# Kernel tuning notes

Hardware: AMD Instinct MI355X
Metric: run time of the kernel (lower is better)

## Reference

```python
import jax, jax.numpy as jnp
import numpy as np

# Elliptical structuring-element sizes (cv2.MORPH_ELLIPSE-like), per init_kwargs.
KERNEL_SIZES = [3, 5, 7]
B, C, H, W = 16, 1, 1024, 1024
_MAX_VAL = 1e4  # kornia's max_val; geodesic border padding uses +-max_val
_EPS = 1e-7     # smp DiceLoss eps


def _ellipse_offsets(k):
    """Offsets (i, j) within a k x k window where the elliptical mask is 1."""
    r = k // 2
    yy, xx = np.mgrid[-r:r + 1, -r:r + 1]
    rr = max(r, 1)
    mask = (xx / rr) ** 2 + (yy / rr) ** 2 <= 1.0 + 1e-9
    return [(i, j) for i in range(k) for j in range(k) if mask[i, j]]


def _morph(x, k, offsets, is_dilation):
    """Flat morphological dilation (max) / erosion (min) over the ellipse support.
    Matches kornia's unfold-based morphology with geodesic border handling,
    but computed as a fused running max/min over static shifted views (no unfold blow-up)."""
    pad = k // 2
    fill = -_MAX_VAL if is_dilation else _MAX_VAL
    xp = jnp.pad(x, ((0, 0), (0, 0), (pad, pad), (pad, pad)), constant_values=fill)
    h, w = x.shape[-2], x.shape[-1]
    op = jnp.maximum if is_dilation else jnp.minimum
    i0, j0 = offsets[0]
    out = xp[..., i0:i0 + h, j0:j0 + w]
    for (i, j) in offsets[1:]:
        out = op(out, xp[..., i:i + h, j:j + w])
    return out


def _dice_loss(pred, target):
    """smp.losses.DiceLoss(mode='binary', from_logits=False): reduce over dims (batch, pixels)."""
    b = pred.shape[0]
    p = pred.reshape(b, 1, -1)
    t = target.reshape(b, 1, -1)
    inter = jnp.sum(p * t, axis=(0, 2))            # [1]
    card = jnp.sum(p + t, axis=(0, 2))             # [1]
    score = 2.0 * inter / jnp.clip(card, _EPS)
    loss = (1.0 - score) * (jnp.sum(t, axis=(0, 2)) > 0)
    return jnp.mean(loss)


def setup_inputs() -> dict:
    key = jax.random.key(0)
    k1, k2 = jax.random.split(key)
    pred = jax.random.uniform(k1, (B, C, H, W), dtype=jnp.float32)
    teacher = jax.random.uniform(k2, (B, C, H, W), dtype=jnp.float32)
    return {"pred_student_prob": pred, "teacher_prob": teacher}


def reference(pred_student_prob, teacher_prob):
    teacher = jax.lax.stop_gradient(teacher_prob)  # .detach()
    total = jnp.float32(0.0)
    for k in KERNEL_SIZES:
        offs = _ellipse_offsets(k)
        obj_dil = _morph(teacher, k, offs, True)
        obj_ero = _morph(teacher, k, offs, False)
        total = total + _dice_loss(pred_student_prob, obj_dil) + _dice_loss(pred_student_prob, obj_ero)
    return total / len(KERNEL_SIZES)
```

## Files before the change

kernel.cpp:

```cpp
#include <hip/hip_runtime.h>

#define H_ 1024
#define W_ 1024
#define B_ 16
#define TH 8
#define STEPS (TH + 6)
#define GX (H_ / TH)
#define NBLK (GX * B_)
#define NACC 13
#define TROW 1032


__device__ __forceinline__ void gl2lds16(const float* g, float* l) {
  __builtin_amdgcn_global_load_lds(
      (const __attribute__((address_space(1))) void*)g,
      (__attribute__((address_space(3))) void*)l,
      16, 0, 0);
}

__global__ __launch_bounds__(256) void k_partials(const float* __restrict__ pred,
                                                  const float* __restrict__ tch,
                                                  float* __restrict__ partials) {
  __shared__ float tbuf[STEPS][TROW];
  __shared__ float red[4][NACC];

  const int tid = threadIdx.x;
  const int n     = blockIdx.y * gridDim.x + blockIdx.x;
  const int b     = n >> 7;
  const int ytile = (n & 7) * 16 + ((n >> 3) & 15);
  const int y0    = ytile * TH;
  const int x0    = tid * 4;
  const int wv    = tid >> 6;
  const float* tb = tch  + (size_t)b * (H_ * W_);
  const float* pb = pred + (size_t)b * (H_ * W_);

#pragma unroll
  for (int s = 0; s < STEPS; ++s) {
    const int t    = y0 + s - 3;
    const int trow = t < 0 ? 0 : (t >= H_ ? H_ - 1 : t);
    gl2lds16(tb + (size_t)trow * W_ + x0, &tbuf[s][4 + (wv << 8)]);
  }
  float4 pv[TH];
#pragma unroll
  for (int j = 0; j < TH; ++j)
    pv[j] = *reinterpret_cast<const float4*>(pb + (size_t)(y0 + j) * W_ + x0);

  __syncthreads();

  float acc[NACC];
#pragma unroll
  for (int j = 0; j < NACC; j++) acc[j] = 0.f;

  float h0q[7][4];
  float h3M[5][4], h3N[5][4];
  float h5M[6][4], h5N[6][4];
  float h7M[4][4], h7N[4][4];

#pragma unroll
  for (int s = 0; s < STEPS; ++s) {
    const float4* t4 = reinterpret_cast<const float4*>(&tbuf[s][x0]);
    const float4 A0 = t4[0], A1 = t4[1], A2 = t4[2];
    float a[12] = {A0.x, A0.y, A0.z, A0.w, A1.x, A1.y, A1.z, A1.w, A2.x, A2.y, A2.z, A2.w};
    if (tid == 0)   { a[0] = a[1] = a[2]  = a[3]  = a[4]; }
    if (tid == 255) { a[8] = a[9] = a[10] = a[11] = a[7]; }

    float QM[8], QN[8];
#pragma unroll
    for (int i = 1; i <= 7; ++i) {
      QM[i] = fmaxf(fmaxf(a[i], a[i + 1]), a[i + 2]);
      QN[i] = fminf(fminf(a[i], a[i + 1]), a[i + 2]);
    }
#pragma unroll
    for (int c = 0; c < 4; ++c) {
      h0q[s % 7][c] = a[c + 4];
      h3M[s % 5][c] = QM[c + 3];
      h3N[s % 5][c] = QN[c + 3];
      h5M[s % 6][c] = fmaxf(QM[c + 2], QM[c + 4]);
      h5N[s % 6][c] = fminf(QN[c + 2], QN[c + 4]);
      h7M[s % 4][c] = fmaxf(fmaxf(QM[c + 1], QM[c + 4]), a[c + 7]);
      h7N[s % 4][c] = fminf(fminf(QN[c + 1], QN[c + 4]), a[c + 7]);
    }

    if (s >= 6) {
      const float4 pq = pv[s - 6];
      const float p[4] = {pq.x, pq.y, pq.z, pq.w};
#pragma unroll
      for (int c = 0; c < 4; ++c) {
        const float d3v = fmaxf(fmaxf(h3M[(s + 2) % 5][c], h0q[(s + 3) % 7][c]), h0q[(s + 5) % 7][c]);
        const float e3v = fminf(fminf(h3N[(s + 2) % 5][c], h0q[(s + 3) % 7][c]), h0q[(s + 5) % 7][c]);

        float d5v = fmaxf(fmaxf(h5M[(s + 3) % 6][c], h3M[(s + 1) % 5][c]), h3M[(s + 3) % 5][c]);
        d5v = fmaxf(fmaxf(d5v, h0q[(s + 2) % 7][c]), h0q[(s + 6) % 7][c]);
        float e5v = fminf(fminf(h5N[(s + 3) % 6][c], h3N[(s + 1) % 5][c]), h3N[(s + 3) % 5][c]);
        e5v = fminf(fminf(e5v, h0q[(s + 2) % 7][c]), h0q[(s + 6) % 7][c]);

        float d7v = fmaxf(fmaxf(h7M[(s + 1) % 4][c], h5M[(s + 2) % 6][c]), h5M[(s + 4) % 6][c]);
        d7v = fmaxf(fmaxf(d7v, h5M[(s + 1) % 6][c]), h5M[(s + 5) % 6][c]);
        d7v = fmaxf(fmaxf(d7v, h0q[(s + 1) % 7][c]), h0q[s % 7][c]);
        float e7v = fminf(fminf(h7N[(s + 1) % 4][c], h5N[(s + 2) % 6][c]), h5N[(s + 4) % 6][c]);
        e7v = fminf(fminf(e7v, h5N[(s + 1) % 6][c]), h5N[(s + 5) % 6][c]);
        e7v = fminf(fminf(e7v, h0q[(s + 1) % 7][c]), h0q[s % 7][c]);

        acc[0]  += p[c];
        acc[1]  += d3v;  acc[2]  = fmaf(p[c], d3v, acc[2]);
        acc[3]  += e3v;  acc[4]  = fmaf(p[c], e3v, acc[4]);
        acc[5]  += d5v;  acc[6]  = fmaf(p[c], d5v, acc[6]);
        acc[7]  += e5v;  acc[8]  = fmaf(p[c], e5v, acc[8]);
        acc[9]  += d7v;  acc[10] = fmaf(p[c], d7v, acc[10]);
        acc[11] += e7v;  acc[12] = fmaf(p[c], e7v, acc[12]);
      }
    }
  }

#pragma unroll
  for (int j = 0; j < NACC; j++) {
    float v = acc[j];
#pragma unroll
    for (int off = 32; off > 0; off >>= 1) v += __shfl_down(v, off, 64);
    acc[j] = v;
  }
  const int lane = tid & 63;
  if (lane == 0) {
#pragma unroll
    for (int j = 0; j < NACC; j++) red[wv][j] = acc[j];
  }
  __syncthreads();
  if (tid == 0) {
    const int bid = n;
#pragma unroll
    for (int j = 0; j < NACC; j++)
      partials[j * NBLK + bid] = red[0][j] + red[1][j] + red[2][j] + red[3][j];
  }
}

__global__ __launch_bounds__(256) void k_final(const float* __restrict__ partials,
                                               float* __restrict__ out) {
  const int tid = threadIdx.x;
  double acc[NACC];
#pragma unroll
  for (int j = 0; j < NACC; j++) acc[j] = 0.0;
#pragma unroll
  for (int k = 0; k < NBLK / 256; k++) {
#pragma unroll
    for (int j = 0; j < NACC; j++)
      acc[j] += (double)partials[j * NBLK + tid + k * 256];
  }
#pragma unroll
  for (int j = 0; j < NACC; j++) {
#pragma unroll
    for (int off = 32; off > 0; off >>= 1) acc[j] += __shfl_down(acc[j], off, 64);
  }
  __shared__ double red[4][NACC];
  const int lane = tid & 63, wv = tid >> 6;
  if (lane == 0) {
#pragma unroll
    for (int j = 0; j < NACC; j++) red[wv][j] = acc[j];
  }
  __syncthreads();
  if (tid == 0) {
    double t_[NACC];
#pragma unroll
    for (int j = 0; j < NACC; j++) t_[j] = red[0][j] + red[1][j] + red[2][j] + red[3][j];
    const double Sp = t_[0];
    double total = 0.0;
#pragma unroll
    for (int k = 0; k < 3; k++) {
      const double Sd = t_[1 + 4 * k], Id = t_[2 + 4 * k];
      const double Se = t_[3 + 4 * k], Ie = t_[4 + 4 * k];
      double cd = Sp + Sd; if (cd < 1e-7) cd = 1e-7;
      double ce = Sp + Se; if (ce < 1e-7) ce = 1e-7;
      total += (1.0 - 2.0 * Id / cd) * (Sd > 0.0 ? 1.0 : 0.0);
      total += (1.0 - 2.0 * Ie / ce) * (Se > 0.0 ? 1.0 : 0.0);
    }
    out[0] = (float)(total / 3.0);
  }
}

extern "C" void kernel_launch(void* const* d_in, const int* in_sizes, int n_in,
                              void* d_out, int out_size, void* d_ws, size_t ws_size,
                              hipStream_t stream) {
  const float* pred = (const float*)d_in[0];
  const float* tch  = (const float*)d_in[1];
  float* partials = (float*)d_ws;

  k_partials<<<dim3(GX, B_), 256, 0, stream>>>(pred, tch, partials);
  k_final<<<1, 256, 0, stream>>>(partials, (float*)d_out);
}
```

Baseline: 147.7 us.

## Load teacher rows directly into register ring buffer, drop LDS staging

Removes the LDS staging of teacher rows and the block-wide barrier. Each of 128 threads now handles 8 columns, loading its own and neighbouring float4 halos from global memory into a 7-row register ring. The morphology switches from horizontal-first to vertical-first partial max/min. Pred rows are loaded inline instead of prefetched, and the block shrinks to 128 threads. The redundant halo loads go through cache. Register pressure from a 7x16 ring plus temporaries may hurt occupancy, and there is less latency hiding without the upfront prefetch.

After: 177.6 us. 1.2x slower.

```diff
diff --git a/kernel.cpp b/kernel.cpp
--- a/kernel.cpp
+++ b/kernel.cpp
@@ -8,106 +8,94 @@
 #define GX (H_ / TH)
 #define NBLK (GX * B_)
 #define NACC 13
-#define TROW 1032
+#define TW 8
+#define BT 128
 
 
-__device__ __forceinline__ void gl2lds16(const float* g, float* l) {
-  __builtin_amdgcn_global_load_lds(
-      (const __attribute__((address_space(1))) void*)g,
-      (__attribute__((address_space(3))) void*)l,
-      16, 0, 0);
-}
-
-__global__ __launch_bounds__(256) void k_partials(const float* __restrict__ pred,
-                                                  const float* __restrict__ tch,
-                                                  float* __restrict__ partials) {
-  __shared__ float tbuf[STEPS][TROW];
-  __shared__ float red[4][NACC];
-
+__global__ __launch_bounds__(BT) void k_partials(const float* __restrict__ pred,
+                                                 const float* __restrict__ tch,
+                                                 float* __restrict__ partials) {
   const int tid = threadIdx.x;
   const int n     = blockIdx.y * gridDim.x + blockIdx.x;
   const int b     = n >> 7;
   const int ytile = (n & 7) * 16 + ((n >> 3) & 15);
   const int y0    = ytile * TH;
-  const int x0    = tid * 4;
-  const int wv    = tid >> 6;
+  const int x0    = tid * TW;
   const float* tb = tch  + (size_t)b * (H_ * W_);
   const float* pb = pred + (size_t)b * (H_ * W_);
-
-#pragma unroll
-  for (int s = 0; s < STEPS; ++s) {
-    const int t    = y0 + s - 3;
-    const int trow = t < 0 ? 0 : (t >= H_ ? H_ - 1 : t);
-    gl2lds16(tb + (size_t)trow * W_ + x0, &tbuf[s][4 + (wv << 8)]);
-  }
-  float4 pv[TH];
-#pragma unroll
-  for (int j = 0; j < TH; ++j)
-    pv[j] = *reinterpret_cast<const float4*>(pb + (size_t)(y0 + j) * W_ + x0);
-
-  __syncthreads();
 
   float acc[NACC];
 #pragma unroll
   for (int j = 0; j < NACC; j++) acc[j] = 0.f;
 
-  float h0q[7][4];
-  float h3M[5][4], h3N[5][4];
-  float h5M[6][4], h5N[6][4];
-  float h7M[4][4], h7N[4][4];
+  float ring[7][16];
 
 #pragma unroll
   for (int s = 0; s < STEPS; ++s) {
-    const float4* t4 = reinterpret_cast<const float4*>(&tbuf[s][x0]);
-    const float4 A0 = t4[0], A1 = t4[1], A2 = t4[2];
-    float a[12] = {A0.x, A0.y, A0.z, A0.w, A1.x, A1.y, A1.z, A1.w, A2.x, A2.y, A2.z, A2.w};
-    if (tid == 0)   { a[0] = a[1] = a[2]  = a[3]  = a[4]; }
-    if (tid == 255) { a[8] = a[9] = a[10] = a[11] = a[7]; }
-
-    float QM[8], QN[8];
-#pragma unroll
-    for (int i = 1; i <= 7; ++i) {
-      QM[i] = fmaxf(fmaxf(a[i], a[i + 1]), a[i + 2]);
-      QN[i] = fminf(fminf(a[i], a[i + 1]), a[i + 2]);
-    }
-#pragma unroll
-    for (int c = 0; c < 4; ++c) {
-      h0q[s % 7][c] = a[c + 4];
-      h3M[s % 5][c] = QM[c + 3];
-      h3N[s % 5][c] = QN[c + 3];
-      h5M[s % 6][c] = fmaxf(QM[c + 2], QM[c + 4]);
-      h5N[s % 6][c] = fminf(QN[c + 2], QN[c + 4]);
-      h7M[s % 4][c] = fmaxf(fmaxf(QM[c + 1], QM[c + 4]), a[c + 7]);
-      h7N[s % 4][c] = fminf(fminf(QN[c + 1], QN[c + 4]), a[c + 7]);
+    {
+      const int t    = y0 + s - 3;
+      const int trow = t < 0 ? 0 : (t >= H_ ? H_ - 1 : t);
+      const float* tr = tb + (size_t)trow * W_ + x0;
+      const float4 v1 = *reinterpret_cast<const float4*>(tr);
+      const float4 v2 = *reinterpret_cast<const float4*>(tr + 4);
+      ring[s % 7][4]  = v1.x; ring[s % 7][5]  = v1.y; ring[s % 7][6]  = v1.z; ring[s % 7][7]  = v1.w;
+      ring[s % 7][8]  = v2.x; ring[s % 7][9]  = v2.y; ring[s % 7][10] = v2.z; ring[s % 7][11] = v2.w;
+      if (tid > 0) {
+        const float4 vl = *reinterpret_cast<const float4*>(tr - 4);
+        ring[s % 7][0] = vl.x; ring[s % 7][1] = vl.y; ring[s % 7][2] = vl.z; ring[s % 7][3] = vl.w;
+      } else {
+        ring[s % 7][0] = ring[s % 7][1] = ring[s % 7][2] = ring[s % 7][3] = v1.x;
+      }
+      if (tid < BT - 1) {
+        const float4 vr = *reinterpret_cast<const float4*>(tr + 8);
+        ring[s % 7][12] = vr.x; ring[s % 7][13] = vr.y; ring[s % 7][14] = vr.z; ring[s % 7][15] = vr.w;
+      } else {
+        ring[s % 7][12] = ring[s % 7][13] = ring[s % 7][14] = ring[s % 7][15] = v2.w;
+      }
     }
 
     if (s >= 6) {
-      const float4 pq = pv[s - 6];
-      const float p[4] = {pq.x, pq.y, pq.z, pq.w};
+      float V3M[16], V3N[16], V5M[16], V5N[16];
 #pragma unroll
-      for (int c = 0; c < 4; ++c) {
-        const float d3v = fmaxf(fmaxf(h3M[(s + 2) % 5][c], h0q[(s + 3) % 7][c]), h0q[(s + 5) % 7][c]);
-        const float e3v = fminf(fminf(h3N[(s + 2) % 5][c], h0q[(s + 3) % 7][c]), h0q[(s + 5) % 7][c]);
+      for (int i = 2; i <= 13; ++i) {
+        const float rm1 = ring[(s + 3) % 7][i], rc = ring[(s + 4) % 7][i], rp1 = ring[(s + 5) % 7][i];
+        V3M[i] = fmaxf(fmaxf(rm1, rc), rp1);
+        V3N[i] = fminf(fminf(rm1, rc), rp1);
+        V5M[i] = fmaxf(fmaxf(V3M[i], ring[(s + 2) % 7][i]), ring[(s + 6) % 7][i]);
+        V5N[i] = fminf(fminf(V3N[i], ring[(s + 2) % 7][i]), ring[(s + 6) % 7][i]);
+      }
+      const float* pr = pb + (size_t)(y0 + s - 6) * W_ + x0;
+      const float4 p1 = *reinterpret_cast<const float4*>(pr);
+      const float4 p2 = *reinterpret_cast<const float4*>(pr + 4);
+      const float p[TW] = {p1.x, p1.y, p1.z, p1.w, p2.x, p2.y, p2.z, p2.w};
+#pragma unroll
+      for (int c = 0; c < TW; ++c) {
+        const int i = c + 4;
+        const float V7M = fmaxf(fmaxf(V5M[i], ring[(s + 1) % 7][i]), ring[s % 7][i]);
+        const float V7N = fminf(fminf(V5N[i], ring[(s + 1) % 7][i]), ring[s % 7][i]);
 
-        float d5v = fmaxf(fmaxf(h5M[(s + 3) % 6][c], h3M[(s + 1) % 5][c]), h3M[(s + 3) % 5][c]);
-        d5v = fmaxf(fmaxf(d5v, h0q[(s + 2) % 7][c]), h0q[(s + 6) % 7][c]);
-        float e5v = fminf(fminf(h5N[(s + 3) % 6][c], h3N[(s + 1) % 5][c]), h3N[(s + 3) % 5][c]);
-        e5v = fminf(fminf(e5v, h0q[(s + 2) % 7][c]), h0q[(s + 6) % 7][c]);
+        const float d3 = fmaxf(fmaxf(V3M[i], ring[(s + 4) % 7][i - 1]), ring[(s + 4) % 7][i + 1]);
+        const float e3 = fminf(fminf(V3N[i], ring[(s + 4) % 7][i - 1]), ring[(s + 4) % 7][i + 1]);
 
-        float d7v = fmaxf(fmaxf(h7M[(s + 1) % 4][c], h5M[(s + 2) % 6][c]), h5M[(s + 4) % 6][c]);
-        d7v = fmaxf(fmaxf(d7v, h5M[(s + 1) % 6][c]), h5M[(s + 5) % 6][c]);
-        d7v = fmaxf(fmaxf(d7v, h0q[(s + 1) % 7][c]), h0q[s % 7][c]);
-        float e7v = fminf(fminf(h7N[(s + 1) % 4][c], h5N[(s + 2) % 6][c]), h5N[(s + 4) % 6][c]);
-        e7v = fminf(fminf(e7v, h5N[(s + 1) % 6][c]), h5N[(s + 5) % 6][c]);
-        e7v = fminf(fminf(e7v, h0q[(s + 1) % 7][c]), h0q[s % 7][c]);
+        float d5 = fmaxf(fmaxf(V5M[i], V3M[i - 1]), V3M[i + 1]);
+        d5 = fmaxf(fmaxf(d5, ring[(s + 4) % 7][i - 2]), ring[(s + 4) % 7][i + 2]);
+        float e5 = fminf(fminf(V5N[i], V3N[i - 1]), V3N[i + 1]);
+        e5 = fminf(fminf(e5, ring[(s + 4) % 7][i - 2]), ring[(s + 4) % 7][i + 2]);
+
+        float d7 = fmaxf(fmaxf(V7M, V5M[i - 1]), V5M[i + 1]);
+        d7 = fmaxf(fmaxf(d7, V5M[i - 2]), V5M[i + 2]);
+        d7 = fmaxf(fmaxf(d7, ring[(s + 4) % 7][i - 3]), ring[(s + 4) % 7][i + 3]);
+        float e7 = fminf(fminf(V7N, V5N[i - 1]), V5N[i + 1]);
+        e7 = fminf(fminf(e7, V5N[i - 2]), V5N[i + 2]);
+        e7 = fminf(fminf(e7, ring[(s + 4) % 7][i - 3]), ring[(s + 4) % 7][i + 3]);
 
         acc[0]  += p[c];
-        acc[1]  += d3v;  acc[2]  = fmaf(p[c], d3v, acc[2]);
-        acc[3]  += e3v;  acc[4]  = fmaf(p[c], e3v, acc[4]);
-        acc[5]  += d5v;  acc[6]  = fmaf(p[c], d5v, acc[6]);
-        acc[7]  += e5v;  acc[8]  = fmaf(p[c], e5v, acc[8]);
-        acc[9]  += d7v;  acc[10] = fmaf(p[c], d7v, acc[10]);
-        acc[11] += e7v;  acc[12] = fmaf(p[c], e7v, acc[12]);
+        acc[1]  += d3;  acc[2]  = fmaf(p[c], d3, acc[2]);
+        acc[3]  += e3;  acc[4]  = fmaf(p[c], e3, acc[4]);
+        acc[5]  += d5;  acc[6]  = fmaf(p[c], d5, acc[6]);
+        acc[7]  += e5;  acc[8]  = fmaf(p[c], e5, acc[8]);
+        acc[9]  += d7;  acc[10] = fmaf(p[c], d7, acc[10]);
+        acc[11] += e7;  acc[12] = fmaf(p[c], e7, acc[12]);
       }
     }
   }
@@ -119,17 +107,17 @@
     for (int off = 32; off > 0; off >>= 1) v += __shfl_down(v, off, 64);
     acc[j] = v;
   }
-  const int lane = tid & 63;
+  __shared__ float red[2][NACC];
+  const int lane = tid & 63, wv = tid >> 6;
   if (lane == 0) {
 #pragma unroll
     for (int j = 0; j < NACC; j++) red[wv][j] = acc[j];
   }
   __syncthreads();
   if (tid == 0) {
-    const int bid = n;
 #pragma unroll
     for (int j = 0; j < NACC; j++)
-      partials[j * NBLK + bid] = red[0][j] + red[1][j] + red[2][j] + red[3][j];
+      partials[j * NBLK + n] = red[0][j] + red[1][j];
   }
 }
 
@@ -183,6 +171,6 @@
   const float* tch  = (const float*)d_in[1];
   float* partials = (float*)d_ws;
 
-  k_partials<<<dim3(GX, B_), 256, 0, stream>>>(pred, tch, partials);
+  k_partials<<<dim3(GX, B_), BT, 0, stream>>>(pred, tch, partials);
   k_final<<<1, 256, 0, stream>>>(partials, (float*)d_out);
 }
```
